# Optimization experiments

Measured on AMD Instinct MI355X. Metric: run time of the kernel, lower is better.

Reference implementation:

```python
import jax, jax.numpy as jnp
import numpy as np

B, N, C = 8, 4096, 768
H, HD = 12, 64          # num_heads, head_dim = C // H
M = HD * 2              # rand_feat_dim
LAM = 0.3
NUM_STEP = 5


def setup_inputs() -> dict:
    key = jax.random.key(0)
    k1, k2, k3, k4 = jax.random.split(key, 4)
    x = jax.random.normal(k1, (B, N, C), dtype=jnp.float32)
    Wqkv = jax.random.normal(k2, (C, 2 * C), dtype=jnp.float32) * 0.02
    Wproj = jax.random.normal(k3, (C, C), dtype=jnp.float32) * 0.02
    bproj = jnp.zeros((C,), dtype=jnp.float32)
    rand_matrix = jax.random.normal(k4, (H, HD, M), dtype=jnp.float32)
    return {"x": x, "Wqkv": Wqkv, "Wproj": Wproj, "bproj": bproj,
            "rand_matrix": rand_matrix}


def _soft(z, t):
    # sign(z) * relu(|z| - t): soft-thresholding (ISTA proximal step)
    return jnp.sign(z) * jax.nn.relu(jnp.abs(z) - t)


def reference(x, Wqkv, Wproj, bproj, rand_matrix):
    Bn, Nn, Cn = x.shape
    Hh, hd, m = rand_matrix.shape
    scale = hd ** (-0.5)

    qkv = x @ Wqkv                                   # [B,N,2C]
    q = qkv[..., :Cn].reshape(Bn, Nn, Hh, hd).transpose(0, 2, 1, 3)  # [B,H,N,hd]
    v = qkv[..., Cn:].reshape(Bn, Nn, Hh, hd).transpose(0, 2, 1, 3)  # [B,H,N,hd]

    # random-feature map: exp(q @ proj - ||q||^2 / 2) / sqrt(m)
    qs = q * scale ** 0.5
    rf = jnp.exp(jnp.einsum('bhnd,hdm->bhnm', qs, rand_matrix)
                 - 0.5 * jnp.sum(qs * qs, axis=-1, keepdims=True)) / m ** 0.5
    # F.normalize(p=2, dim=-2): normalize over the sequence axis
    qn = rf / jnp.maximum(jnp.linalg.norm(rf, axis=-2, keepdims=True), 1e-12)

    kk = jnp.einsum('bhnm,bhnp->bhmp', qn, qn)       # [B,H,m,m]
    kv = jnp.einsum('bhnm,bhnd->bhmd', qn, v)        # [B,H,m,hd]

    # Lipschitz bound: max row L1 norm of kk, detached
    L = jax.lax.stop_gradient(
        jnp.max(jnp.sum(jnp.abs(kk), axis=-1), axis=-1))[..., None, None] + 1.0

    # unrolled ISTA soft-thresholding loop
    s = _soft(kv, LAM)
    for _ in range(NUM_STEP):
        s = _soft(s - (kk @ s - kv) / L, LAM / L)

    out = jnp.einsum('bhnm,bhmd->bhnd', qn, s)       # [B,H,N,hd]
    out = out.transpose(0, 2, 1, 3).reshape(Bn, Nn, Cn)
    return out @ Wproj + bproj
```

## Files before the change

### kernel.cpp

```cpp
#include <hip/hip_runtime.h>


typedef __attribute__((ext_vector_type(8))) short bf16x8;
typedef __attribute__((ext_vector_type(4))) float f32x4;

#define GLD16(gptr, lptr)                                                              \
  __builtin_amdgcn_global_load_lds((const __attribute__((address_space(1))) void*)(gptr), \
                                   (__attribute__((address_space(3))) void*)(lptr), 16, 0, 0)

__device__ __forceinline__ unsigned short f2bf(float f) {
  union { float f; unsigned int u; } v; v.f = f;
  unsigned int r = v.u + 0x7fffu + ((v.u >> 16) & 1u);
  return (unsigned short)(r >> 16);
}
__device__ __forceinline__ float bf2f(unsigned short s) {
  union { unsigned int u; float f; } v; v.u = ((unsigned int)s) << 16;
  return v.f;
}
__device__ __forceinline__ float rn_of(float css) {
  return 1.f / fmaxf(sqrtf(css), 1e-12f);
}

template<int ITERS>
__device__ __forceinline__ void gemm256_core(
    const unsigned short* __restrict__ A,
    const unsigned short* __restrict__ B,
    int ldk,
    f32x4 (&acc)[8][4],
    unsigned short* smem) {
  const int tid = threadIdx.x;
  const int lane = tid & 63, wave = tid >> 6;
  const int l16 = lane & 15, quad = lane >> 4;
  const int wr = wave >> 2, wc = wave & 3;
  const int rsw = l16 & 7;

#pragma unroll
  for (int i = 0; i < 8; i++)
#pragma unroll
    for (int j = 0; j < 4; j++)
#pragma unroll
      for (int r = 0; r < 4; r++) acc[i][j][r] = 0.f;

  const int srow0 = tid >> 3, sc0 = ((tid & 7) ^ (srow0 & 7)) << 3;
  const int srow1 = (tid + 512) >> 3, sc1 = ((tid & 7) ^ (srow1 & 7)) << 3;
  const int dstw = wave * 512;

  auto stageA = [&](int T, int h) {
    const unsigned short* g = A + (long)(h * 128) * ldk + T * 64;
    unsigned short* d = smem + (T & 1) * 32768 + h * 8192 + dstw;
    GLD16(g + (long)srow0 * ldk + sc0, d);
    GLD16(g + (long)srow1 * ldk + sc1, d + 4096);
  };
  auto stageB = [&](int T, int h) {
    const unsigned short* g = B + (long)(h * 128) * ldk + T * 64;
    unsigned short* d = smem + (T & 1) * 32768 + 16384 + h * 8192 + dstw;
    GLD16(g + (long)srow0 * ldk + sc0, d);
    GLD16(g + (long)srow1 * ldk + sc1, d + 4096);
  };

  bf16x8 af[4][2], bn[4][2];

  auto rdA_ks = [&](int b, int mh, int ks) {
    const unsigned short* p = smem + b * 32768 + wr * 8192 + (mh * 64 + l16) * 64;
#pragma unroll
    for (int ii = 0; ii < 4; ii++)
      af[ii][ks] = *(const bf16x8*)(p + ii * 1024 + (((ks * 4 + quad) ^ rsw) << 3));
  };
  auto rdB_ks = [&](int b, int ks) {
    const unsigned short* p = smem + b * 32768 + 16384 + (wc >> 1) * 8192 +
                              ((wc & 1) * 64 + l16) * 64;
#pragma unroll
    for (int jj = 0; jj < 4; jj++)
      bn[jj][ks] = *(const bf16x8*)(p + jj * 1024 + (((ks * 4 + quad) ^ rsw) << 3));
  };

  auto mma16 = [&](int mh, int ks) {
    __builtin_amdgcn_s_setprio(1);
#pragma unroll
    for (int ii = 0; ii < 4; ii++)
#pragma unroll
      for (int jj = 0; jj < 4; jj++)
        acc[mh * 4 + ii][jj] = __builtin_amdgcn_mfma_f32_16x16x32_bf16(
            af[ii][ks], bn[jj][ks], acc[mh * 4 + ii][jj], 0, 0, 0);
    __builtin_amdgcn_s_setprio(0);
  };

#define FENCE asm volatile("" ::: "memory")
#define SGB __builtin_amdgcn_sched_barrier(0)
#define LGKM(n) asm volatile("s_waitcnt lgkmcnt(" #n ")" ::: "memory")

  stageA(0, 0); stageA(0, 1); stageB(0, 0); stageB(0, 1);
  stageB(1, 0); stageB(1, 1);
  asm volatile("s_waitcnt vmcnt(4)" ::: "memory");
  __builtin_amdgcn_s_barrier();

#pragma unroll 1
  for (int i = 0; i < ITERS; i++) {
    const int u = 2 * i;
    const bool more = (i + 1 < ITERS);
    stageA(u + 1, 0);
    rdB_ks(0, 0); rdA_ks(0, 0, 0);
    SGB;
    rdB_ks(0, 1); rdA_ks(0, 0, 1);
    FENCE; __builtin_amdgcn_s_barrier();
    LGKM(8); SGB;
    mma16(0, 0);
    LGKM(0); SGB;
    mma16(0, 1);
    FENCE; __builtin_amdgcn_s_barrier();
    stageA(u + 1, 1);
    if (more) stageB(u + 2, 0);
    rdA_ks(0, 1, 0);
    SGB;
    rdA_ks(0, 1, 1);
    FENCE; __builtin_amdgcn_s_barrier();
    LGKM(4); SGB;
    mma16(1, 0);
    LGKM(0); SGB;
    mma16(1, 1);
    if (more) { asm volatile("s_waitcnt vmcnt(2)" ::: "memory"); }
    else      { asm volatile("s_waitcnt vmcnt(0)" ::: "memory"); }
    FENCE; __builtin_amdgcn_s_barrier();
    if (more) { stageB(u + 2, 1); stageA(u + 2, 0); stageA(u + 2, 1); }
    rdB_ks(1, 0); rdA_ks(1, 0, 0);
    SGB;
    rdB_ks(1, 1); rdA_ks(1, 0, 1);
    FENCE; __builtin_amdgcn_s_barrier();
    LGKM(8); SGB;
    mma16(0, 0);
    LGKM(0); SGB;
    mma16(0, 1);
    FENCE; __builtin_amdgcn_s_barrier();
    if (more) { stageB(u + 3, 0); stageB(u + 3, 1); }
    rdA_ks(1, 1, 0);
    SGB;
    rdA_ks(1, 1, 1);
    FENCE; __builtin_amdgcn_s_barrier();
    LGKM(4); SGB;
    mma16(1, 0);
    LGKM(0); SGB;
    mma16(1, 1);
    if (more) { asm volatile("s_waitcnt vmcnt(4)" ::: "memory"); }
    FENCE; __builtin_amdgcn_s_barrier();
  }
#undef FENCE
#undef SGB
#undef LGKM
}

__global__ __launch_bounds__(256) void k_convert_bf16(const float* __restrict__ in,
                                                      unsigned short* __restrict__ out, long n4) {
  long i = (long)blockIdx.x * 256 + threadIdx.x;
  if (i < n4) {
    float4 v = ((const float4*)in)[i];
    unsigned short o[4] = {f2bf(v.x), f2bf(v.y), f2bf(v.z), f2bf(v.w)};
    ((uint2*)out)[i] = *(uint2*)o;
  }
}

__global__ __launch_bounds__(256) void k_transpose_tiled(const float* __restrict__ in,
                                                         unsigned short* __restrict__ out,
                                                         int R, int C, float scale) {
  __shared__ float t[32][33];
  const float* ib = in + (long)blockIdx.z * R * C;
  unsigned short* ob = out + (long)blockIdx.z * R * C;
  int c0 = blockIdx.x * 32, r0 = blockIdx.y * 32;
  int tx = threadIdx.x & 31, ty = threadIdx.x >> 5;
#pragma unroll
  for (int k = 0; k < 32; k += 8)
    t[ty + k][tx] = ib[(long)(r0 + ty + k) * C + c0 + tx];
  __syncthreads();
#pragma unroll
  for (int k = 0; k < 32; k += 8)
    ob[(long)(c0 + ty + k) * R + r0 + tx] = f2bf(t[tx][ty + k] * scale);
}

__global__ __launch_bounds__(512, 2) void k_gemm_qkv256(const unsigned short* __restrict__ xbf,
                                                        const unsigned short* __restrict__ wqkvT,
                                                        unsigned short* __restrict__ q,
                                                        unsigned short* __restrict__ vT) {
  __shared__ __align__(16) unsigned short smem[65536];
  f32x4 acc[8][4];
  const int L = blockIdx.x;
  const int xcd = L & 7, slot = L >> 3;
  const int rt = xcd * 16 + slot / 6;
  const int ct = slot % 6;
  gemm256_core<6>(xbf + (long)rt * 256 * 768, wqkvT + (long)ct * 256 * 768, 768, acc, smem);

  const int tid = threadIdx.x, lane = tid & 63, wave = tid >> 6;
  const int l16 = lane & 15, quad = lane >> 4;
  const int wr = wave >> 2, wc = wave & 3;
  const int b = rt >> 4;
  const int nbase = (rt & 15) * 256;
  if (ct < 3) {
#pragma unroll
    for (int i = 0; i < 8; i++)
#pragma unroll
      for (int j = 0; j < 4; j++) {
        int col = ct * 256 + wc * 64 + j * 16 + l16;
        int h = col >> 6, d = col & 63;
#pragma unroll
        for (int r = 0; r < 4; r++) {
          int n = nbase + wr * 128 + i * 16 + quad * 4 + r;
          q[((long)(b * 12 + h) * 4096 + n) * 64 + d] = f2bf(acc[i][j][r]);
        }
      }
  } else {
    unsigned short* pool = smem;
    for (int hh = 0; hh < 2; hh++) {
      __syncthreads();
      if (wr == hh) {
#pragma unroll
        for (int i = 0; i < 8; i++)
#pragma unroll
          for (int j = 0; j < 4; j++)
#pragma unroll
            for (int r = 0; r < 4; r++)
              pool[(wc * 64 + j * 16 + l16) * 136 + i * 16 + quad * 4 + r] = f2bf(acc[i][j][r]);
      }
      __syncthreads();
#pragma unroll
      for (int it = 0; it < 8; it++) {
        int chunk = it * 512 + tid;
        int col = chunk >> 4, ng = chunk & 15;
        uint4 val = *(const uint4*)&pool[col * 136 + ng * 8];
        int vcol = (ct - 3) * 256 + col;
        int h = vcol >> 6, d = vcol & 63;
        long n = nbase + hh * 128 + ng * 8;
        *(uint4*)&vT[((long)(b * 12 + h) * 64 + d) * 4096 + n] = val;
      }
    }
  }
}

__global__ __launch_bounds__(256) void k_gemm_rf(const unsigned short* __restrict__ q,
                                                 const unsigned short* __restrict__ rmT,
                                                 unsigned short* __restrict__ qnT,
                                                 float* __restrict__ colss) {
  __shared__ __align__(16) unsigned short smem[16384];
  __shared__ float hnp[256];
  __shared__ float css[128];
  unsigned short* Asm = smem;
  unsigned short* Bsm = smem + 8192;
  unsigned short* pool = smem;
  f32x4 acc[4][4];
  const int nt = blockIdx.x, bh = blockIdx.y, h = bh % 12;
  const int tid = threadIdx.x, lane = tid & 63, wave = tid >> 6;
  const int l16 = lane & 15, quad = lane >> 4;
  const int wm = (wave >> 1) * 64, wn = (wave & 1) * 64;
  const int fsw = (l16 >> 1) & 3;
  const unsigned short* Aq = q + ((long)bh * 4096 + nt * 128) * 64;
  const unsigned short* Brm = rmT + (long)h * 8192;

#pragma unroll
  for (int c = 0; c < 4; c++) {
    int chunk = c * 256 + tid;
    int row = chunk >> 3, ko8 = chunk & 7;
    int kc = ko8 >> 2;
    int c2s = (ko8 & 3) ^ ((row >> 1) & 3);
    *(uint4*)(Asm + kc * 4096 + row * 32 + c2s * 8) = *(const uint4*)(Aq + (long)row * 64 + ko8 * 8);
    *(uint4*)(Bsm + kc * 4096 + row * 32 + c2s * 8) = *(const uint4*)(Brm + (long)row * 64 + ko8 * 8);
  }
  for (int i = tid; i < 128; i += 256) css[i] = 0.f;
  __syncthreads();
  {
    const unsigned short* ap = Asm + (tid & 1) * 4096 + (tid >> 1) * 32;
    float ssum = 0.f;
#pragma unroll
    for (int e = 0; e < 32; e++) { float f = bf2f(ap[e]); ssum += f * f; }
    hnp[tid] = ssum;
  }
#pragma unroll
  for (int i = 0; i < 4; i++)
#pragma unroll
    for (int j = 0; j < 4; j++)
#pragma unroll
      for (int r = 0; r < 4; r++) acc[i][j][r] = 0.f;
#pragma unroll
  for (int kc = 0; kc < 2; kc++) {
    bf16x8 af[4], bfr[4];
#pragma unroll
    for (int i = 0; i < 4; i++)
      af[i] = *(const bf16x8*)(Asm + kc * 4096 + (wm + i * 16 + l16) * 32 + ((quad ^ fsw) * 8));
#pragma unroll
    for (int j = 0; j < 4; j++)
      bfr[j] = *(const bf16x8*)(Bsm + kc * 4096 + (wn + j * 16 + l16) * 32 + ((quad ^ fsw) * 8));
#pragma unroll
    for (int i = 0; i < 4; i++)
#pragma unroll
      for (int j = 0; j < 4; j++)
        acc[i][j] = __builtin_amdgcn_mfma_f32_16x16x32_bf16(af[i], bfr[j], acc[i][j], 0, 0, 0);
  }
  __syncthreads();
  float hnv[4][4];
#pragma unroll
  for (int i = 0; i < 4; i++)
#pragma unroll
    for (int r = 0; r < 4; r++) {
      int row = wm + i * 16 + quad * 4 + r;
      hnv[i][r] = 0.0625f * (hnp[2 * row] + hnp[2 * row + 1]);
    }
#pragma unroll
  for (int j = 0; j < 4; j++) {
    int col = wn + j * 16 + l16;
    float cp = 0.f;
#pragma unroll
    for (int i = 0; i < 4; i++)
#pragma unroll
      for (int r = 0; r < 4; r++) {
        float v = __expf(acc[i][j][r] - hnv[i][r]) * 0.08838834764831845f;
        acc[i][j][r] = v;
        cp += v * v;
      }
    atomicAdd(&css[col], cp);
  }
  __syncthreads();
  for (int i = tid; i < 128; i += 256) atomicAdd(&colss[bh * 128 + i], css[i]);
  for (int hh = 0; hh < 2; hh++) {
    __syncthreads();
    if ((wave >> 1) == hh) {
#pragma unroll
      for (int i = 0; i < 4; i++)
#pragma unroll
        for (int j = 0; j < 4; j++)
#pragma unroll
          for (int r = 0; r < 4; r++)
            pool[(i * 16 + quad * 4 + r) * 134 + wn + j * 16 + l16] = f2bf(acc[i][j][r]);
    }
    __syncthreads();
#pragma unroll
    for (int c = 0; c < 4; c++) {
      int chunk = tid + c * 256;
      int m = chunk >> 3, nj = (chunk & 7) * 8;
      unsigned short o[8];
#pragma unroll
      for (int e = 0; e < 8; e++) o[e] = pool[(nj + e) * 134 + m];
      *(uint4*)&qnT[((long)bh * 128 + m) * 4096 + nt * 128 + hh * 64 + nj] = *(uint4*)o;
    }
  }
}

__global__ __launch_bounds__(256) void k_gemm_kkkv(const unsigned short* __restrict__ qnT,
                                                   const unsigned short* __restrict__ vT,
                                                   const float* __restrict__ colss,
                                                   unsigned short* __restrict__ kkp) {
  __shared__ __align__(16) unsigned short As[128 * 32], Bs[64 * 32];
  f32x4 acc[4][6];
  const int ks = blockIdx.x, bh = blockIdx.y;
  const unsigned short* A = qnT + (long)bh * 128 * 4096 + ks * 512;
  const unsigned short* B1 = vT + (long)bh * 64 * 4096 + ks * 512;
  const int tid = threadIdx.x, lane = tid & 63, wave = tid >> 6;
  const int l16 = lane & 15, quad = lane >> 4;
  const int wm = (wave >> 1) * 64, wn = (wave & 1) * 96;
  const int arow = tid >> 2;
  const int akos = (((tid & 3) ^ ((arow >> 1) & 3)) << 3);
  const int fsw = (l16 >> 1) & 3;
#pragma unroll
  for (int i = 0; i < 4; i++)
#pragma unroll
    for (int j = 0; j < 6; j++)
#pragma unroll
      for (int r = 0; r < 4; r++) acc[i][j][r] = 0.f;
  for (int k0 = 0; k0 < 512; k0 += 32) {
    __syncthreads();
    GLD16(A + (long)arow * 4096 + k0 + akos, As + wave * 512);
    GLD16(A + (long)(arow + 64) * 4096 + k0 + akos, As + 2048 + wave * 512);
    GLD16(B1 + (long)arow * 4096 + k0 + akos, Bs + wave * 512);
    __syncthreads();
    bf16x8 af[4], bfr[6];
#pragma unroll
    for (int i = 0; i < 4; i++)
      af[i] = *(const bf16x8*)(As + (wm + i * 16 + l16) * 32 + ((quad ^ fsw) * 8));
#pragma unroll
    for (int j = 0; j < 6; j++) {
      int row = wn + j * 16 + l16;
      const unsigned short* rp = (row < 128) ? (As + row * 32) : (Bs + (row - 128) * 32);
      bfr[j] = *(const bf16x8*)(rp + ((quad ^ fsw) * 8));
    }
#pragma unroll
    for (int i = 0; i < 4; i++)
#pragma unroll
      for (int j = 0; j < 6; j++)
        acc[i][j] = __builtin_amdgcn_mfma_f32_16x16x32_bf16(af[i], bfr[j], acc[i][j], 0, 0, 0);
  }
  unsigned short* dst = kkp + ((long)ks * 96 + bh) * 24576;
  float rnr[4][4];
#pragma unroll
  for (int i = 0; i < 4; i++)
#pragma unroll
    for (int r = 0; r < 4; r++)
      rnr[i][r] = rn_of(colss[bh * 128 + wm + i * 16 + quad * 4 + r]);
#pragma unroll
  for (int j = 0; j < 6; j++) {
    int col = wn + j * 16 + l16;
    float rnc = (col < 128) ? rn_of(colss[bh * 128 + col]) : 1.f;
#pragma unroll
    for (int i = 0; i < 4; i++)
#pragma unroll
      for (int r = 0; r < 4; r++) {
        int row = wm + i * 16 + quad * 4 + r;
        dst[row * 192 + col] = f2bf(acc[i][j][r] * rnr[i][r] * rnc);
      }
  }
}

__global__ __launch_bounds__(256) void k_ista(const unsigned short* __restrict__ kkp,
                                              const float* __restrict__ colss,
                                              unsigned short* __restrict__ sT) {
  __shared__ __align__(16) unsigned short kks[128 * 144];
  __shared__ __align__(16) unsigned short ssT[64 * 144];
  __shared__ float kvs[128 * 64];
  __shared__ float red[128];
  __shared__ float rns[128];
  const int tid = threadIdx.x, lane = tid & 63, wave = tid >> 6;
  const int l16 = lane & 15, quad = lane >> 4;
  const int wm = (wave >> 1) * 64, wn = (wave & 1) * 32;
  const int bh = blockIdx.x;
  const unsigned short* base = kkp + (long)bh * 24576;
  for (int idx = tid; idx < 3072; idx += 256) {
    int m = idx / 24, c8 = idx % 24;
    float f[8] = {0.f, 0.f, 0.f, 0.f, 0.f, 0.f, 0.f, 0.f};
#pragma unroll
    for (int ks = 0; ks < 8; ks++) {
      union { uint4 u; unsigned short s[8]; } u;
      u.u = *(const uint4*)(base + (long)ks * 2359296 + m * 192 + c8 * 8);
#pragma unroll
      for (int e = 0; e < 8; e++) f[e] += bf2f(u.s[e]);
    }
    if (c8 < 16) {
#pragma unroll
      for (int e = 0; e < 8; e++) kks[m * 144 + c8 * 8 + e] = f2bf(f[e]);
    } else {
#pragma unroll
      for (int e = 0; e < 8; e++) kvs[m * 64 + (c8 - 16) * 8 + e] = f[e];
    }
  }
  __syncthreads();
  float kv[4][2][4];
#pragma unroll
  for (int i = 0; i < 4; i++)
#pragma unroll
    for (int j = 0; j < 2; j++)
#pragma unroll
      for (int r = 0; r < 4; r++) {
        int m = wm + i * 16 + quad * 4 + r, d = wn + j * 16 + l16;
        kv[i][j][r] = kvs[m * 64 + d];
      }
  if (tid < 128) {
    float rs = 0.f;
    const unsigned short* rp = kks + tid * 144;
    for (int p = 0; p < 128; p++) rs += fabsf(bf2f(rp[p]));
    red[tid] = rs;
    rns[tid] = rn_of(colss[bh * 128 + tid]);
  }
  __syncthreads();
  for (int o = 64; o > 0; o >>= 1) {
    if (tid < o) red[tid] = fmaxf(red[tid], red[tid + o]);
    __syncthreads();
  }
  const float L = red[0] + 1.f;
  const float invL = 1.f / L;
  const float lamL = 0.3f * invL;
  float sreg[4][2][4];
#pragma unroll
  for (int i = 0; i < 4; i++)
#pragma unroll
    for (int j = 0; j < 2; j++)
#pragma unroll
      for (int r = 0; r < 4; r++) {
        float z = kv[i][j][r];
        float az = fabsf(z) - 0.3f;
        float s = az > 0.f ? copysignf(az, z) : 0.f;
        sreg[i][j][r] = s;
        ssT[(wn + j * 16 + l16) * 144 + wm + i * 16 + quad * 4 + r] = f2bf(s);
      }
  for (int step = 0; step < 5; step++) {
    __syncthreads();
    f32x4 acc[4][2];
#pragma unroll
    for (int i = 0; i < 4; i++)
#pragma unroll
      for (int j = 0; j < 2; j++)
#pragma unroll
        for (int r = 0; r < 4; r++) acc[i][j][r] = 0.f;
#pragma unroll
    for (int kc = 0; kc < 4; kc++) {
      bf16x8 af[4], bfj[2];
#pragma unroll
      for (int i = 0; i < 4; i++)
        af[i] = *(const bf16x8*)(kks + (wm + i * 16 + l16) * 144 + kc * 32 + quad * 8);
#pragma unroll
      for (int j = 0; j < 2; j++)
        bfj[j] = *(const bf16x8*)(ssT + (wn + j * 16 + l16) * 144 + kc * 32 + quad * 8);
#pragma unroll
      for (int i = 0; i < 4; i++)
#pragma unroll
        for (int j = 0; j < 2; j++)
          acc[i][j] = __builtin_amdgcn_mfma_f32_16x16x32_bf16(af[i], bfj[j], acc[i][j], 0, 0, 0);
    }
    __syncthreads();
#pragma unroll
    for (int i = 0; i < 4; i++)
#pragma unroll
      for (int j = 0; j < 2; j++)
#pragma unroll
        for (int r = 0; r < 4; r++) {
          float z = sreg[i][j][r] - (acc[i][j][r] - kv[i][j][r]) * invL;
          float az = fabsf(z) - lamL;
          float s = az > 0.f ? copysignf(az, z) : 0.f;
          sreg[i][j][r] = s;
          ssT[(wn + j * 16 + l16) * 144 + wm + i * 16 + quad * 4 + r] = f2bf(s);
        }
  }
#pragma unroll
  for (int i = 0; i < 4; i++)
#pragma unroll
    for (int j = 0; j < 2; j++)
#pragma unroll
      for (int r = 0; r < 4; r++) {
        int m = wm + i * 16 + quad * 4 + r, d = wn + j * 16 + l16;
        sT[(long)bh * 8192 + d * 128 + m] = f2bf(sreg[i][j][r] * rns[m]);
      }
}

__global__ __launch_bounds__(256) void k_gemm_attn(const unsigned short* __restrict__ qnT,
                                                   const unsigned short* __restrict__ sT,
                                                   unsigned short* __restrict__ attn) {
  __shared__ __align__(16) unsigned short As2[4352];
  __shared__ __align__(16) unsigned short Bs[64 * 32];
  f32x4 acc[4][2];
  const int nt = blockIdx.x, bh = blockIdx.y;
  const int b = bh / 12, h = bh % 12;
  const int tid = threadIdx.x, lane = tid & 63, wave = tid >> 6;
  const int l16 = lane & 15, quad = lane >> 4;
  const int wm = (wave >> 1) * 64, wn = (wave & 1) * 32;
  const int fsw = (l16 >> 1) & 3;
#pragma unroll
  for (int i = 0; i < 4; i++)
#pragma unroll
    for (int j = 0; j < 2; j++)
#pragma unroll
      for (int r = 0; r < 4; r++) acc[i][j][r] = 0.f;
  for (int k0 = 0; k0 < 128; k0 += 32) {
    __syncthreads();
#pragma unroll
    for (int it = 0; it < 3; it++) {
      if (it < 2 || tid < 32) {
        int c = it * 256 + tid;
        int p = (c * 241) >> 12;
        int nh = c - p * 17;
        int k = ((p & 7) << 2) + (p >> 3);
        int n8 = (nh < 16 ? nh : 15) << 3;
        const unsigned short* gp = qnT + ((long)bh * 128 + k0 + k) * 4096 + nt * 128 + n8;
        GLD16(gp, As2 + (it * 256 + wave * 64) * 8);
      }
    }
    {
      int dd = tid >> 2;
      int ko = (((tid & 3) ^ ((dd >> 1) & 3)) * 8);
      const unsigned short* gp = sT + ((long)bh * 64 + dd) * 128 + k0 + ko;
      GLD16(gp, Bs + wave * 512);
    }
    __syncthreads();
    bf16x8 af[4], bfr[2];
#pragma unroll
    for (int i = 0; i < 4; i++) {
      union { bf16x8 v; unsigned short s[8]; } u;
#pragma unroll
      for (int e = 0; e < 8; e++) {
        int p = ((e & 3) << 3) + (quad << 1) + (e >> 2);
        u.s[e] = As2[p * 136 + wm + i * 16 + l16];
      }
      af[i] = u.v;
    }
#pragma unroll
    for (int j = 0; j < 2; j++)
      bfr[j] = *(const bf16x8*)&Bs[(wn + j * 16 + l16) * 32 + ((quad ^ fsw) * 8)];
#pragma unroll
    for (int i = 0; i < 4; i++)
#pragma unroll
      for (int j = 0; j < 2; j++)
        acc[i][j] = __builtin_amdgcn_mfma_f32_16x16x32_bf16(af[i], bfr[j], acc[i][j], 0, 0, 0);
  }
#pragma unroll
  for (int i = 0; i < 4; i++)
#pragma unroll
    for (int j = 0; j < 2; j++)
#pragma unroll
      for (int r = 0; r < 4; r++) {
        int n = nt * 128 + wm + i * 16 + quad * 4 + r;
        int dd = wn + j * 16 + l16;
        attn[((long)b * 4096 + n) * 768 + h * 64 + dd] = f2bf(acc[i][j][r]);
      }
}

__global__ __launch_bounds__(512, 2) void k_gemm_proj256(const unsigned short* __restrict__ attn,
                                                         const unsigned short* __restrict__ wprojT,
                                                         const float* __restrict__ bias,
                                                         float* __restrict__ out) {
  __shared__ __align__(16) unsigned short smem[65536];
  f32x4 acc[8][4];
  const int L = blockIdx.x;
  const int xcd = L & 7, slot = L >> 3;
  const int rt = xcd * 16 + slot / 3;
  const int ct = slot % 3;
  gemm256_core<6>(attn + (long)rt * 256 * 768, wprojT + (long)ct * 256 * 768, 768, acc, smem);
  const int tid = threadIdx.x, lane = tid & 63, wave = tid >> 6;
  const int l16 = lane & 15, quad = lane >> 4;
  const int wr = wave >> 2, wc = wave & 3;
  const long row0 = (long)rt * 256 + wr * 128;
#pragma unroll
  for (int i = 0; i < 8; i++)
#pragma unroll
    for (int j = 0; j < 4; j++) {
      int col = ct * 256 + wc * 64 + j * 16 + l16;
      float bv = bias[col];
#pragma unroll
      for (int r = 0; r < 4; r++) {
        long row = row0 + i * 16 + quad * 4 + r;
        out[row * 768 + col] = acc[i][j][r] + bv;
      }
    }
}

extern "C" void kernel_launch(void* const* d_in, const int* in_sizes, int n_in,
                              void* d_out, int out_size, void* d_ws, size_t ws_size,
                              hipStream_t stream) {
  const float* x = (const float*)d_in[0];
  const float* Wqkv = (const float*)d_in[1];
  const float* Wproj = (const float*)d_in[2];
  const float* bproj = (const float*)d_in[3];
  const float* rm = (const float*)d_in[4];
  float* out = (float*)d_out;

  size_t o = 0;
  char* wsb = (char*)d_ws;
  auto take = [&](size_t b) { char* p = wsb + o; o += b; return p; };
  unsigned short* wqkvT = (unsigned short*)take(2359296);
  unsigned short* wprojT = (unsigned short*)take(1179648);
  unsigned short* rmT = (unsigned short*)take(196608);
  unsigned short* q = (unsigned short*)take(50331648);
  unsigned short* vT = (unsigned short*)take(50331648);
  float* colss = (float*)take(49152);
  unsigned short* sT = (unsigned short*)take(1572864);
  if (ws_size < o) return;

  unsigned short* xbf = (unsigned short*)d_out;
  unsigned short* qnT = (unsigned short*)d_out;
  unsigned short* kkp = q;
  unsigned short* attnbf = q;

  hipMemsetAsync(colss, 0, 49152, stream);

  k_convert_bf16<<<24576, 256, 0, stream>>>(x, xbf, 6291456L);
  k_transpose_tiled<<<dim3(48, 24, 1), 256, 0, stream>>>(Wqkv, wqkvT, 768, 1536, 1.0f);
  k_transpose_tiled<<<dim3(24, 24, 1), 256, 0, stream>>>(Wproj, wprojT, 768, 768, 1.0f);
  k_transpose_tiled<<<dim3(4, 2, 12), 256, 0, stream>>>(rm, rmT, 64, 128, 0.3535533905932738f);
  k_gemm_qkv256<<<768, 512, 0, stream>>>(xbf, wqkvT, q, vT);
  k_gemm_rf<<<dim3(32, 96), 256, 0, stream>>>(q, rmT, qnT, colss);
  k_gemm_kkkv<<<dim3(8, 96), 256, 0, stream>>>(qnT, vT, colss, kkp);
  k_ista<<<96, 256, 0, stream>>>(kkp, colss, sT);
  k_gemm_attn<<<dim3(32, 96), 256, 0, stream>>>(qnT, sT, attnbf);
  k_gemm_proj256<<<384, 512, 0, stream>>>(attnbf, wprojT, bproj, out);
}
```

Baseline: 453.2 us.

## Split ISTA partial-sum reduction into parallel kernel and shrink proj GEMM tiles

Moves the reduction of split-K kk/kv partials out of the 96-block ISTA kernel into a separate kernel launched over 384 blocks. The ISTA kernel then only loads the reduced results. The projection GEMM also switches from 256x256 tiles over 384 blocks to 128x256 tiles over 768 blocks, using a new double-buffered core. The aim is to fill more CUs in both phases, at the cost of an extra launch, an extra round trip of the reduced data through global memory, and less reuse per tile in the GEMM.

```diff
diff --git a/kernel.cpp b/kernel.cpp
--- a/kernel.cpp
+++ b/kernel.cpp
@@ -142,6 +142,99 @@
     mma16(1, 1);
     if (more) { asm volatile("s_waitcnt vmcnt(4)" ::: "memory"); }
     FENCE; __builtin_amdgcn_s_barrier();
+  }
+#undef FENCE
+#undef SGB
+#undef LGKM
+}
+
+template<int NT>
+__device__ __forceinline__ void gemm128x256_core(
+    const unsigned short* __restrict__ A,
+    const unsigned short* __restrict__ B,
+    int ldk,
+    f32x4 (&acc)[4][4],
+    unsigned short* smem) {
+  const int tid = threadIdx.x;
+  const int lane = tid & 63, wave = tid >> 6;
+  const int l16 = lane & 15, quad = lane >> 4;
+  const int wr = wave >> 2, wc = wave & 3;
+  const int rsw = l16 & 7;
+
+#pragma unroll
+  for (int m = 0; m < 4; m++)
+#pragma unroll
+    for (int n = 0; n < 4; n++)
+#pragma unroll
+      for (int r = 0; r < 4; r++) acc[m][n][r] = 0.f;
+
+  const int srow0 = tid >> 3, sc0 = ((tid & 7) ^ (srow0 & 7)) << 3;
+  const int srow1 = (tid + 512) >> 3, sc1 = ((tid & 7) ^ (srow1 & 7)) << 3;
+  const int dstw = wave * 512;
+
+  auto stage = [&](int T) {
+    unsigned short* d = smem + (T & 1) * 24576;
+    const unsigned short* gA = A + T * 64;
+    const unsigned short* gB = B + T * 64;
+    GLD16(gA + (long)srow0 * ldk + sc0, d + dstw);
+    GLD16(gA + (long)srow1 * ldk + sc1, d + 4096 + dstw);
+    GLD16(gB + (long)srow0 * ldk + sc0, d + 8192 + dstw);
+    GLD16(gB + (long)srow1 * ldk + sc1, d + 8192 + 4096 + dstw);
+    GLD16(gB + (long)(srow0 + 128) * ldk + sc0, d + 16384 + dstw);
+    GLD16(gB + (long)(srow1 + 128) * ldk + sc1, d + 16384 + 4096 + dstw);
+  };
+
+  bf16x8 af[4][2], bn[4][2];
+
+  auto rdA_ks = [&](int b, int ks) {
+    const unsigned short* p = smem + b * 24576 + (wr * 64 + l16) * 64;
+#pragma unroll
+    for (int m = 0; m < 4; m++)
+      af[m][ks] = *(const bf16x8*)(p + m * 1024 + (((ks * 4 + quad) ^ rsw) << 3));
+  };
+  auto rdB_ks = [&](int b, int ks) {
+    const unsigned short* p = smem + b * 24576 + 8192 + (wc * 64 + l16) * 64;
+#pragma unroll
+    for (int n = 0; n < 4; n++)
+      bn[n][ks] = *(const bf16x8*)(p + n * 1024 + (((ks * 4 + quad) ^ rsw) << 3));
+  };
+
+  auto mma16 = [&](int ks) {
+    __builtin_amdgcn_s_setprio(1);
+#pragma unroll
+    for (int m = 0; m < 4; m++)
+#pragma unroll
+      for (int n = 0; n < 4; n++)
+        acc[m][n] = __builtin_amdgcn_mfma_f32_16x16x32_bf16(
+            af[m][ks], bn[n][ks], acc[m][n], 0, 0, 0);
+    __builtin_amdgcn_s_setprio(0);
+  };
+
+#define FENCE asm volatile("" ::: "memory")
+#define SGB __builtin_amdgcn_sched_barrier(0)
+#define LGKM(n) asm volatile("s_waitcnt lgkmcnt(" #n ")" ::: "memory")
+
+  stage(0); stage(1);
+  asm volatile("s_waitcnt vmcnt(6)" ::: "memory");
+  __builtin_amdgcn_s_barrier();
+
+#pragma unroll 1
+  for (int t = 0; t < NT; t++) {
+    const int b = t & 1;
+    rdA_ks(b, 0); rdB_ks(b, 0);
+    SGB;
+    rdA_ks(b, 1); rdB_ks(b, 1);
+    LGKM(8); SGB;
+    mma16(0);
+    LGKM(0); SGB;
+    mma16(1);
+    FENCE; __builtin_amdgcn_s_barrier();
+    if (t + 2 < NT) stage(t + 2);
+    if (t + 1 < NT) {
+      if (t + 2 < NT) { asm volatile("s_waitcnt vmcnt(6)" ::: "memory"); }
+      else            { asm volatile("s_waitcnt vmcnt(0)" ::: "memory"); }
+      FENCE; __builtin_amdgcn_s_barrier();
+    }
   }
 #undef FENCE
 #undef SGB
@@ -404,9 +497,41 @@
   }
 }
 
-__global__ __launch_bounds__(256) void k_ista(const unsigned short* __restrict__ kkp,
-                                              const float* __restrict__ colss,
-                                              unsigned short* __restrict__ sT) {
+__global__ __launch_bounds__(256) void k_red(const unsigned short* __restrict__ kkp,
+                                             unsigned short* __restrict__ kkred,
+                                             float* __restrict__ kvred) {
+  const int g = blockIdx.x, bh = blockIdx.y;
+  const int tid = threadIdx.x;
+  const unsigned short* base = kkp + (long)bh * 24576 + (long)(g * 32) * 192;
+#pragma unroll
+  for (int c = 0; c < 3; c++) {
+    int idx = c * 256 + tid;
+    int m = idx / 24, c8 = idx % 24;
+    float f[8] = {0.f, 0.f, 0.f, 0.f, 0.f, 0.f, 0.f, 0.f};
+#pragma unroll
+    for (int ks = 0; ks < 8; ks++) {
+      union { uint4 u; unsigned short s[8]; } u;
+      u.u = *(const uint4*)(base + (long)ks * 2359296 + m * 192 + c8 * 8);
+#pragma unroll
+      for (int e = 0; e < 8; e++) f[e] += bf2f(u.s[e]);
+    }
+    long row = (long)bh * 128 + g * 32 + m;
+    if (c8 < 16) {
+      unsigned short o[8];
+#pragma unroll
+      for (int e = 0; e < 8; e++) o[e] = f2bf(f[e]);
+      *(uint4*)&kkred[row * 128 + c8 * 8] = *(uint4*)o;
+    } else {
+      *(float4*)&kvred[row * 64 + (c8 - 16) * 8] = make_float4(f[0], f[1], f[2], f[3]);
+      *(float4*)&kvred[row * 64 + (c8 - 16) * 8 + 4] = make_float4(f[4], f[5], f[6], f[7]);
+    }
+  }
+}
+
+__global__ __launch_bounds__(256) void k_ista2(const unsigned short* __restrict__ kkred,
+                                               const float* __restrict__ kvred,
+                                               const float* __restrict__ colss,
+                                               unsigned short* __restrict__ sT) {
   __shared__ __align__(16) unsigned short kks[128 * 144];
   __shared__ __align__(16) unsigned short ssT[64 * 144];
   __shared__ float kvs[128 * 64];
@@ -416,24 +541,15 @@
   const int l16 = lane & 15, quad = lane >> 4;
   const int wm = (wave >> 1) * 64, wn = (wave & 1) * 32;
   const int bh = blockIdx.x;
-  const unsigned short* base = kkp + (long)bh * 24576;
-  for (int idx = tid; idx < 3072; idx += 256) {
-    int m = idx / 24, c8 = idx % 24;
-    float f[8] = {0.f, 0.f, 0.f, 0.f, 0.f, 0.f, 0.f, 0.f};
-#pragma unroll
-    for (int ks = 0; ks < 8; ks++) {
-      union { uint4 u; unsigned short s[8]; } u;
-      u.u = *(const uint4*)(base + (long)ks * 2359296 + m * 192 + c8 * 8);
-#pragma unroll
-      for (int e = 0; e < 8; e++) f[e] += bf2f(u.s[e]);
-    }
-    if (c8 < 16) {
-#pragma unroll
-      for (int e = 0; e < 8; e++) kks[m * 144 + c8 * 8 + e] = f2bf(f[e]);
-    } else {
-#pragma unroll
-      for (int e = 0; e < 8; e++) kvs[m * 64 + (c8 - 16) * 8 + e] = f[e];
-    }
+  for (int idx = tid; idx < 2048; idx += 256) {
+    int m = idx >> 4, c8 = idx & 15;
+    uint4 v = *(const uint4*)(kkred + ((long)bh * 128 + m) * 128 + c8 * 8);
+    *(uint4*)&kks[m * 144 + c8 * 8] = v;
+  }
+  for (int idx = tid; idx < 2048; idx += 256) {
+    int m = idx >> 4, c4 = idx & 15;
+    float4 v = *(const float4*)(kvred + ((long)bh * 128 + m) * 64 + c4 * 4);
+    *(float4*)&kvs[m * 64 + c4 * 4] = v;
   }
   __syncthreads();
   float kv[4][2][4];
@@ -594,31 +710,32 @@
       }
 }
 
-__global__ __launch_bounds__(512, 2) void k_gemm_proj256(const unsigned short* __restrict__ attn,
+__global__ __launch_bounds__(512, 2) void k_gemm_proj128(const unsigned short* __restrict__ attn,
                                                          const unsigned short* __restrict__ wprojT,
                                                          const float* __restrict__ bias,
                                                          float* __restrict__ out) {
-  __shared__ __align__(16) unsigned short smem[65536];
-  f32x4 acc[8][4];
+  __shared__ __align__(16) unsigned short smem[49152];
+  f32x4 acc[4][4];
   const int L = blockIdx.x;
   const int xcd = L & 7, slot = L >> 3;
-  const int rt = xcd * 16 + slot / 3;
+  const int rt = xcd * 32 + slot / 3;
   const int ct = slot % 3;
-  gemm256_core<6>(attn + (long)rt * 256 * 768, wprojT + (long)ct * 256 * 768, 768, acc, smem);
+  gemm128x256_core<12>(attn + (long)rt * 128 * 768, wprojT + (long)ct * 256 * 768, 768,
+                       acc, smem);
   const int tid = threadIdx.x, lane = tid & 63, wave = tid >> 6;
   const int l16 = lane & 15, quad = lane >> 4;
   const int wr = wave >> 2, wc = wave & 3;
-  const long row0 = (long)rt * 256 + wr * 128;
-#pragma unroll
-  for (int i = 0; i < 8; i++)
-#pragma unroll
-    for (int j = 0; j < 4; j++) {
-      int col = ct * 256 + wc * 64 + j * 16 + l16;
+  const long row0 = (long)rt * 128 + wr * 64;
+#pragma unroll
+  for (int m = 0; m < 4; m++)
+#pragma unroll
+    for (int n = 0; n < 4; n++) {
+      int col = ct * 256 + wc * 64 + n * 16 + l16;
       float bv = bias[col];
 #pragma unroll
       for (int r = 0; r < 4; r++) {
-        long row = row0 + i * 16 + quad * 4 + r;
-        out[row * 768 + col] = acc[i][j][r] + bv;
+        long row = row0 + m * 16 + quad * 4 + r;
+        out[row * 768 + col] = acc[m][n][r] + bv;
       }
     }
 }
@@ -649,6 +766,8 @@
   unsigned short* qnT = (unsigned short*)d_out;
   unsigned short* kkp = q;
   unsigned short* attnbf = q;
+  unsigned short* kkred = vT;
+  float* kvred = (float*)(vT + 1572864);
 
   hipMemsetAsync(colss, 0, 49152, stream);
 
@@ -659,7 +778,8 @@
   k_gemm_qkv256<<<768, 512, 0, stream>>>(xbf, wqkvT, q, vT);
   k_gemm_rf<<<dim3(32, 96), 256, 0, stream>>>(q, rmT, qnT, colss);
   k_gemm_kkkv<<<dim3(8, 96), 256, 0, stream>>>(qnT, vT, colss, kkp);
-  k_ista<<<96, 256, 0, stream>>>(kkp, colss, sT);
+  k_red<<<dim3(4, 96), 256, 0, stream>>>(kkp, kkred, kvred);
+  k_ista2<<<96, 256, 0, stream>>>(kkred, kvred, colss, sT);
   k_gemm_attn<<<dim3(32, 96), 256, 0, stream>>>(qnT, sT, attnbf);
-  k_gemm_proj256<<<384, 512, 0, stream>>>(attnbf, wprojT, bproj, out);
-}
+  k_gemm_proj128<<<768, 512, 0, stream>>>(attnbf, wprojT, bproj, out);
+}
```

Result: no change. 450.5 us (-0.6%).
